# Performance work log

Measured on AMD Instinct MI355X. Metric: run time of the kernel, lower is better.

The kernel has to match this reference:

```python
import jax, jax.numpy as jnp
import numpy as np

B, M, H, R = 4096, 4, 1024, 10
MID, D3 = 512, 3 * H  # gate MLP mid = max(32, H//2)
AUDIO = 1
OTHERS = (0, 2, 3)


def _ln(x, w, b):
    m = jnp.mean(x, axis=-1, keepdims=True)
    v = jnp.mean((x - m) ** 2, axis=-1, keepdims=True)
    return (x - m) * jax.lax.rsqrt(v + 1e-5) * w + b


def _gate(t, s, lw, lb, w1, b1, w2, b2):
    feat = jnp.concatenate([t, s, jnp.abs(t - s)], axis=-1)  # [..., 3H]
    h = jax.nn.gelu(_ln(feat, lw, lb) @ w1.T + b1, approximate=False)
    return jax.nn.sigmoid(h @ w2.T + b2)  # [..., 1]


def setup_inputs() -> dict:
    key = jax.random.key(0)
    ks = jax.random.split(key, 16)
    xn = lambda k, shp, fan: jax.random.normal(k, shp, jnp.float32) * (1.0 / np.sqrt(fan))
    inp = {
        'tokens': jax.random.normal(ks[0], (B, M, H), jnp.float32),
        'token_mask': jax.random.randint(ks[1], (B, M), 0, 2) > 0,
        # gate_other: LayerNorm(3H) -> Linear(3H,MID) -> GELU -> Linear(MID,1)
        'ln_go_w': jnp.ones((D3,), jnp.float32), 'ln_go_b': jnp.zeros((D3,), jnp.float32),
        'go_w1': xn(ks[2], (MID, D3), D3), 'go_b1': jnp.zeros((MID,), jnp.float32),
        'go_w2': xn(ks[3], (1, MID), MID), 'go_b2': jnp.zeros((1,), jnp.float32),
        # gate_audio
        'ln_ga_w': jnp.ones((D3,), jnp.float32), 'ln_ga_b': jnp.zeros((D3,), jnp.float32),
        'ga_w1': xn(ks[4], (MID, D3), D3), 'ga_b1': jnp.zeros((MID,), jnp.float32),
        'ga_w2': xn(ks[5], (1, MID), MID), 'ga_b2': jnp.zeros((1,), jnp.float32),
        'a2o_w': xn(ks[6], (H, H), H), 'o2a_w': xn(ks[7], (H, H), H),
        'ln_o_w': jnp.ones((H,), jnp.float32), 'ln_o_b': jnp.zeros((H,), jnp.float32),
        'ln_a_w': jnp.ones((H,), jnp.float32), 'ln_a_b': jnp.zeros((H,), jnp.float32),
        # LMF
        'factors': jax.random.normal(ks[8], (M, R, H + 1, H), jnp.float32) * np.sqrt(2.0 / (H + 1 + H)),
        'rank_w': jax.random.normal(ks[9], (R,), jnp.float32) * 0.02,
        'lmf_bias': jnp.zeros((H,), jnp.float32),
        'out_ln1_w': jnp.ones((H,), jnp.float32), 'out_ln1_b': jnp.zeros((H,), jnp.float32),
        'out_w': xn(ks[10], (H, H), H), 'out_b': jnp.zeros((H,), jnp.float32),
        'out_ln2_w': jnp.ones((H,), jnp.float32), 'out_ln2_b': jnp.zeros((H,), jnp.float32),
    }
    return inp


def reference(tokens, token_mask, ln_go_w, ln_go_b, go_w1, go_b1, go_w2, go_b2,
              ln_ga_w, ln_ga_b, ga_w1, ga_b1, ga_w2, ga_b2, a2o_w, o2a_w,
              ln_o_w, ln_o_b, ln_a_w, ln_a_b, factors, rank_w, lmf_bias,
              out_ln1_w, out_ln1_b, out_w, out_b, out_ln2_w, out_ln2_b):
    mask_f = token_mask.astype(tokens.dtype)  # [B, M]
    oidx = jnp.asarray(OTHERS)

    # ---- AudioGuidedResidualMixer (eval mode) ----
    audio = tokens[:, AUDIO]                          # [B, H]
    audio_valid = token_mask[:, AUDIO]                # [B]
    others = tokens[:, oidx] * mask_f[:, oidx, None]  # [B, 3, H] (masked targets)
    src = jnp.broadcast_to(audio[:, None, :], others.shape)
    g = _gate(others, src, ln_go_w, ln_go_b, go_w1, go_b1, go_w2, go_b2)  # [B,3,1]
    a2o = audio @ a2o_w.T                                                  # [B, H]
    upd = _ln(others + g * a2o[:, None, :], ln_o_w, ln_o_b)
    pair_valid = token_mask[:, oidx] & audio_valid[:, None]                # [B, 3]
    others_new = jnp.where(pair_valid[..., None], upd, others) * mask_f[:, oidx, None]

    w_o = mask_f[:, oidx, None]
    denom = jnp.clip(w_o.sum(axis=1), 1.0, None)
    others_mean = (others_new * w_o).sum(axis=1) / denom                   # [B, H]
    aum = audio_valid & token_mask[:, oidx].any(axis=1)                    # [B]
    g_a = _gate(audio, others_mean, ln_ga_w, ln_ga_b, ga_w1, ga_b1, ga_w2, ga_b2)
    o2a = others_mean @ o2a_w.T
    mixed_audio = jnp.where(aum[:, None],
                            _ln(audio + g_a * o2a, ln_a_w, ln_a_b),
                            audio * mask_f[:, AUDIO, None])
    mixed = jnp.stack([others_new[:, 0], mixed_audio, others_new[:, 1], others_new[:, 2]],
                      axis=1) * mask_f[..., None]                          # [B, M, H]

    # ---- LowRankMultiplicativeFusion ----
    one = jnp.ones((mixed.shape[0], M, 1), mixed.dtype)
    x_aug = jnp.concatenate([one, mixed], axis=-1)                         # [B, M, H+1]
    z = jnp.einsum('bmd,mrdh->bmrh', x_aug, factors)                       # [B, M, R, H]
    z = jnp.where(token_mask[:, :, None, None], z, jnp.ones((), z.dtype))
    rank_tensor = jnp.prod(z, axis=1)                                      # [B, R, H]
    fused = jnp.einsum('brh,r->bh', rank_tensor, rank_w) + lmf_bias
    h = _ln(fused, out_ln1_w, out_ln1_b)
    h = jax.nn.gelu(h @ out_w.T + out_b, approximate=False)
    return _ln(h, out_ln2_w, out_ln2_b)                                    # [B, H]
```

## Files before the change

### kernel.cpp

```cpp
#include <hip/hip_runtime.h>
#include <math.h>

#define BB 4096
#define HH 1024
#define RR 10
#define MIDD 512
#define D3 3072

typedef __bf16 bf16x8 __attribute__((ext_vector_type(8)));
typedef __bf16 bf16x4 __attribute__((ext_vector_type(4)));
typedef float f32x4 __attribute__((ext_vector_type(4)));

__device__ __forceinline__ float waveSum(float v){
#pragma unroll
  for(int o=32;o>0;o>>=1) v += __shfl_down(v,o,64);
  return v;
}
__device__ __forceinline__ float blockSum256(float v, float* sc){
  v = waveSum(v);
  __syncthreads();
  if((threadIdx.x & 63)==0) sc[threadIdx.x>>6] = v;
  __syncthreads();
  return sc[0]+sc[1]+sc[2]+sc[3];
}
__device__ __forceinline__ float gelu_f(float x){
  return 0.5f*x*(1.0f+erff(x*0.70710678118654752f));
}
__device__ __forceinline__ void gl_lds16(const void* g, void* lds){
  __builtin_amdgcn_global_load_lds((const __attribute__((address_space(1))) unsigned int*)g,
                                   (__attribute__((address_space(3))) unsigned int*)lds,
                                   16, 0, 0);
}

__global__ void convw_k(const float* __restrict__ s0, __bf16* __restrict__ d0, int n0,
                        const float* __restrict__ s1, __bf16* __restrict__ d1, int n1,
                        const float* __restrict__ s2, __bf16* __restrict__ d2, int n2,
                        const float* __restrict__ s3, __bf16* __restrict__ d3, int n3,
                        const float* __restrict__ s4, __bf16* __restrict__ d4, int n4){
  long i = ((long)blockIdx.x*256 + threadIdx.x)*4;
  const float* s; __bf16* d;
  if(i<n0){ s=s0; d=d0; }
  else { i-=n0; if(i<n1){ s=s1; d=d1; }
  else { i-=n1; if(i<n2){ s=s2; d=d2; }
  else { i-=n2; if(i<n3){ s=s3; d=d3; }
  else { i-=n3; if(i>=n4) return; s=s4; d=d4; } } } }
  float4 v=*(const float4*)(s+i);
  bf16x4 o; o[0]=(__bf16)v.x; o[1]=(__bf16)v.y; o[2]=(__bf16)v.z; o[3]=(__bf16)v.w;
  *(bf16x4*)(d+i)=o;
}

__global__ void feat_go_k(const float* __restrict__ tokens, const int* __restrict__ mask,
                          const float* __restrict__ lnw, const float* __restrict__ lnb,
                          __bf16* __restrict__ featGo, __bf16* __restrict__ audioB){
  int row=blockIdx.x; int b=row/3; int j=row-b*3; int oj=(j==0)?0:(j+1);
  const float* to=tokens+((size_t)b*4+oj)*HH;
  const float* ta=tokens+((size_t)b*4+1)*HH;
  float mo = mask[b*4+oj]?1.f:0.f;
  int tid=threadIdx.x;
  __shared__ float sc[4];
  float ov[4], av[4], dv[4]; float s=0.f,s2=0.f;
#pragma unroll
  for(int p=0;p<4;p++){
    int h=tid+p*256;
    float o=to[h]*mo, a=ta[h], d=fabsf(o-a);
    ov[p]=o; av[p]=a; dv[p]=d;
    s+=o+a+d; s2+=o*o+a*a+d*d;
  }
  s=blockSum256(s,sc); s2=blockSum256(s2,sc);
  float mean=s/(float)D3, rstd=rsqrtf(s2/(float)D3-mean*mean+1e-5f);
  __bf16* fr = featGo + (size_t)row*D3;
#pragma unroll
  for(int p=0;p<4;p++){
    int h=tid+p*256;
    fr[h]       =(__bf16)((ov[p]-mean)*rstd*lnw[h]+lnb[h]);
    fr[1024+h]  =(__bf16)((av[p]-mean)*rstd*lnw[1024+h]+lnb[1024+h]);
    fr[2048+h]  =(__bf16)((dv[p]-mean)*rstd*lnw[2048+h]+lnb[2048+h]);
    if(j==0) audioB[(size_t)b*HH+h]=(__bf16)av[p];
  }
}

__global__ void feat_ga_k(const float* __restrict__ tokens, const float* __restrict__ omean,
                          const float* __restrict__ lnw, const float* __restrict__ lnb,
                          __bf16* __restrict__ featGa){
  int b=blockIdx.x; int tid=threadIdx.x;
  const float* ta=tokens+((size_t)b*4+1)*HH;
  const float* so=omean+(size_t)b*HH;
  __shared__ float sc[4];
  float tv[4], sv[4], dv[4]; float s=0.f,s2=0.f;
#pragma unroll
  for(int p=0;p<4;p++){
    int h=tid+p*256;
    float a=ta[h], o=so[h], d=fabsf(a-o);
    tv[p]=a; sv[p]=o; dv[p]=d;
    s+=a+o+d; s2+=a*a+o*o+d*d;
  }
  s=blockSum256(s,sc); s2=blockSum256(s2,sc);
  float mean=s/(float)D3, rstd=rsqrtf(s2/(float)D3-mean*mean+1e-5f);
  __bf16* fr = featGa + (size_t)b*D3;
#pragma unroll
  for(int p=0;p<4;p++){
    int h=tid+p*256;
    fr[h]     =(__bf16)((tv[p]-mean)*rstd*lnw[h]+lnb[h]);
    fr[1024+h]=(__bf16)((sv[p]-mean)*rstd*lnw[1024+h]+lnb[1024+h]);
    fr[2048+h]=(__bf16)((dv[p]-mean)*rstd*lnw[2048+h]+lnb[2048+h]);
  }
}

template<int ACT>
__launch_bounds__(256, 4)
__global__ void gemm_nt_mfma(const __bf16* __restrict__ A, int lda,
                             const __bf16* __restrict__ Bm, int ldb,
                             const float* __restrict__ bias,
                             float* __restrict__ C, int ldc, int K){
  __shared__ __align__(16) __bf16 As[3*2048];
  __shared__ __align__(16) __bf16 Bs[3*4096];
  const int tid=threadIdx.x, l=tid&63, w=tid>>6;
  const int wr=w>>1, wc=w&1;
  const int quad=l>>4, lr16=l&15;

  const int nbx = gridDim.x;
  const int flat = blockIdx.x + nbx*blockIdx.y;
  const int chunk = (nbx*gridDim.y)>>3;
  const int nid = (flat&7)*chunk + (flat>>3);
  const int bx = nid % nbx, by = nid / nbx;
  const int row0=by*64, col0=bx*128;

  const int srow=l>>2, sq=(l&3)^((l>>3)&3);
  const int nsteps = K>>5;

  const __bf16* pa  = A  + (size_t)(row0 + w*16       + srow)*lda + sq*8;
  const __bf16* pb0 = Bm + (size_t)(col0 + w*16       + srow)*ldb + sq*8;
  const __bf16* pb1 = Bm + (size_t)(col0 + (w+4)*16   + srow)*ldb + sq*8;
  __bf16* da  = As + ((size_t)w*64     + l)*8;
  __bf16* db0 = Bs + ((size_t)w*64     + l)*8;
  __bf16* db1 = Bs + ((size_t)(w+4)*64 + l)*8;

  auto stage=[&](int s,int bi){
    int k0 = s*32;
    gl_lds16(pa  + k0, da  + bi*2048);
    gl_lds16(pb0 + k0, db0 + bi*4096);
    gl_lds16(pb1 + k0, db1 + bi*4096);
  };

  f32x4 acc[2][4];
  f32x4 zerov={0.f,0.f,0.f,0.f};
#pragma unroll
  for(int i=0;i<2;i++)
#pragma unroll
    for(int j=0;j<4;j++) acc[i][j]=zerov;

  stage(0,0);
  stage(1,1);
  asm volatile("s_waitcnt vmcnt(3)" ::: "memory");
  __builtin_amdgcn_s_barrier();

  int cur=0;
  for(int step=0; step<nsteps; ++step){
    const __bf16* Ab = As + cur*2048;
    const __bf16* Bb = Bs + cur*4096;
    bf16x8 af[2], bg[4];
#pragma unroll
    for(int fi=0;fi<2;fi++){
      int R = wr*32 + fi*16 + lr16;
      af[fi]=*(const bf16x8*)(Ab + R*32 + ((quad^(R>>1))&3)*8);
    }
#pragma unroll
    for(int fj=0;fj<4;fj++){
      int N = wc*64 + fj*16 + lr16;
      bg[fj]=*(const bf16x8*)(Bb + N*32 + ((quad^(N>>1))&3)*8);
    }
    if(step+2<nsteps){
      int bi = cur + 2; if(bi>=3) bi-=3;
      stage(step+2, bi);
    }
    __builtin_amdgcn_s_setprio(1);
#pragma unroll
    for(int fi=0;fi<2;fi++)
#pragma unroll
      for(int fj=0;fj<4;fj++)
        acc[fi][fj]=__builtin_amdgcn_mfma_f32_16x16x32_bf16(af[fi],bg[fj],acc[fi][fj],0,0,0);
    __builtin_amdgcn_s_setprio(0);
    asm volatile("s_waitcnt lgkmcnt(0)" ::: "memory");
    if(step < nsteps-2) asm volatile("s_waitcnt vmcnt(3)" ::: "memory");
    else                asm volatile("s_waitcnt vmcnt(0)" ::: "memory");
    __builtin_amdgcn_s_barrier();
    cur = (cur+1==3)?0:cur+1;
  }

  float bv[4];
#pragma unroll
  for(int fj=0;fj<4;fj++) bv[fj] = (ACT==1)? bias[col0+wc*64+fj*16+lr16] : 0.f;
#pragma unroll
  for(int fi=0;fi<2;fi++){
#pragma unroll
    for(int reg=0;reg<4;reg++){
      int row=row0+wr*32+fi*16+quad*4+reg;
#pragma unroll
      for(int fj=0;fj<4;fj++){
        int col=col0+wc*64+fj*16+lr16;
        float v=acc[fi][fj][reg];
        if(ACT==1) v=gelu_f(v+bv[fj]);
        C[(size_t)row*ldc+col]=v;
      }
    }
  }
}

__global__ void gate_reduce_k(const float* __restrict__ Hx, const float* __restrict__ w2,
                              const float* __restrict__ b2, float* __restrict__ g, int cols){
  int row=blockIdx.x;
  float s=0.f;
  for(int c=threadIdx.x;c<cols;c+=64) s += Hx[(size_t)row*cols+c]*w2[c];
  s=waveSum(s);
  if(threadIdx.x==0) g[row]=1.f/(1.f+expf(-(s+b2[0])));
}

__global__ void others_k(const float* __restrict__ tokens, const int* __restrict__ mask,
                         const float* __restrict__ g, const float* __restrict__ a2o,
                         const float* __restrict__ lnw, const float* __restrict__ lnb,
                         __bf16* __restrict__ mixedB, float* __restrict__ omean,
                         __bf16* __restrict__ omeanB){
  int b=blockIdx.x, tid=threadIdx.x;
  __shared__ float sc[4];
  float ma = mask[b*4+1]?1.f:0.f;
  float a2[4];
#pragma unroll
  for(int p=0;p<4;p++) a2[p]=a2o[(size_t)b*HH+tid+p*256];
  float sum[4]={0,0,0,0}; float cnt=0.f;
  for(int j=0;j<3;j++){
    int oj=(j==0)?0:(j+1);
    float mo=mask[b*4+oj]?1.f:0.f; cnt+=mo;
    float gv=g[b*3+j];
    float t[4], ov[4]; float s=0.f,s2=0.f;
#pragma unroll
    for(int p=0;p<4;p++){
      int h=tid+p*256;
      float o=tokens[((size_t)b*4+oj)*HH+h]*mo;
      ov[p]=o; t[p]=o+gv*a2[p];
      s+=t[p]; s2+=t[p]*t[p];
    }
    s=blockSum256(s,sc); s2=blockSum256(s2,sc);
    float mean=s/1024.f, rstd=rsqrtf(s2/1024.f-mean*mean+1e-5f);
    float pv=mo*ma;
#pragma unroll
    for(int p=0;p<4;p++){
      int h=tid+p*256;
      float upd=(t[p]-mean)*rstd*lnw[h]+lnb[h];
      float on=((pv>0.5f)?upd:ov[p])*mo;
      mixedB[(size_t)b*4096 + (size_t)oj*HH + h]=(__bf16)on;
      sum[p]+=on*mo;
    }
  }
  float denom=fmaxf(cnt,1.f);
#pragma unroll
  for(int p=0;p<4;p++){
    float v=sum[p]/denom;
    omean[(size_t)b*HH+tid+p*256]=v;
    omeanB[(size_t)b*HH+tid+p*256]=(__bf16)v;
  }
}

__global__ void audio_k(const float* __restrict__ tokens, const int* __restrict__ mask,
                        const float* __restrict__ g_a, const float* __restrict__ o2a,
                        const float* __restrict__ lnw, const float* __restrict__ lnb,
                        __bf16* __restrict__ mixedB){
  int b=blockIdx.x, tid=threadIdx.x;
  __shared__ float sc[4];
  int ma_i=mask[b*4+1];
  int any = mask[b*4+0]|mask[b*4+2]|mask[b*4+3];
  bool aum = (ma_i!=0) && (any!=0);
  float ma = ma_i?1.f:0.f;
  float gv=g_a[b];
  const float* ta = tokens + ((size_t)b*4+1)*HH;
  float av[4], t[4]; float s=0.f,s2=0.f;
#pragma unroll
  for(int p=0;p<4;p++){
    int h=tid+p*256;
    av[p]=ta[h];
    t[p]=av[p]+gv*o2a[(size_t)b*HH+h];
    s+=t[p]; s2+=t[p]*t[p];
  }
  s=blockSum256(s,sc); s2=blockSum256(s2,sc);
  float mean=s/1024.f, rstd=rsqrtf(s2/1024.f-mean*mean+1e-5f);
#pragma unroll
  for(int p=0;p<4;p++){
    int h=tid+p*256;
    float u=(t[p]-mean)*rstd*lnw[h]+lnb[h];
    float outv = aum ? u : av[p]*ma;
    mixedB[(size_t)b*4096 + HH + h]=(__bf16)(outv*ma);
  }
}

__global__ void transpose_factors_k(const float* __restrict__ factors,
                                    __bf16* __restrict__ factT){
  __shared__ float T[64][65];
  int mr = blockIdx.z;
  int d0 = blockIdx.y*64, h0 = blockIdx.x*64;
  int t = threadIdx.x;
  int rr = t>>4, cc = (t&15)*4;
  const float* src = factors + ((size_t)mr*1025 + 1 + d0)*1024 + h0;
#pragma unroll
  for(int q=0;q<4;q++){
    float4 v = *(const float4*)(src + (size_t)(q*16+rr)*1024 + cc);
    T[q*16+rr][cc]=v.x; T[q*16+rr][cc+1]=v.y; T[q*16+rr][cc+2]=v.z; T[q*16+rr][cc+3]=v.w;
  }
  __syncthreads();
  __bf16* dst = factT + ((size_t)mr*1024 + h0)*1024 + d0;
#pragma unroll
  for(int q=0;q<4;q++){
    int hr = q*16 + rr;
    bf16x4 o;
    o[0]=(__bf16)T[cc][hr];   o[1]=(__bf16)T[cc+1][hr];
    o[2]=(__bf16)T[cc+2][hr]; o[3]=(__bf16)T[cc+3][hr];
    *(bf16x4*)(dst + (size_t)hr*1024 + cc) = o;
  }
}

__launch_bounds__(256, 2)
__global__ void gemm_lmf_mfma(const __bf16* __restrict__ mixedB,
                              const __bf16* __restrict__ factT,
                              const float* __restrict__ factors,
                              const int* __restrict__ mask,
                              float* __restrict__ P){
  __shared__ __align__(16) __bf16 As[3*4096];
  __shared__ __align__(16) __bf16 Bs[3*4096];
  __shared__ float Mskf[4][128];
  __shared__ float F0s[4][128];
  const int tid = threadIdx.x;
  const int l = tid & 63, w = tid >> 6;
  const int wr = w >> 1, wc = w & 1;
  const int quad = l >> 4, lr16 = l & 15;

  const int flat = blockIdx.x + 8*(blockIdx.y + 32*blockIdx.z);
  const int nid  = (flat & 7)*320 + (flat >> 3);
  const int bx   = nid & 7;
  const int rest = nid >> 3;
  const int by   = rest & 31;
  const int r    = rest >> 5;
  const int row0 = by * 128, col0 = bx * 128;

  const int srow = l >> 2;
  const int sq   = (l & 3) ^ ((l >> 3) & 3);

  for(int i = tid; i < 512; i += 256){
    int mm = i >> 7, rl = i & 127;
    Mskf[mm][rl] = mask[(row0 + rl)*4 + mm] ? 1.f : 0.f;
    F0s[mm][rl]  = factors[(size_t)(mm*RR + r)*1025*1024 + col0 + rl];
  }

  const __bf16* pa0 = mixedB + (size_t)(row0 + w*16     + srow)*4096 + sq*8;
  const __bf16* pa1 = mixedB + (size_t)(row0 + (w+4)*16 + srow)*4096 + sq*8;
  const __bf16* pb0 = factT + ((size_t)r*1024 + col0 + w*16     + srow)*1024 + sq*8;
  const __bf16* pb1 = factT + ((size_t)r*1024 + col0 + (w+4)*16 + srow)*1024 + sq*8;
  __bf16* da0 = As + ((size_t)w*64     + l)*8;
  __bf16* da1 = As + ((size_t)(w+4)*64 + l)*8;
  __bf16* db0 = Bs + ((size_t)w*64     + l)*8;
  __bf16* db1 = Bs + ((size_t)(w+4)*64 + l)*8;

  auto stage = [&](int s, int bi){
    int mm = s >> 5; int k0 = (s & 31)*32;
    size_t ao = (size_t)mm*1024 + k0;
    size_t bo = (size_t)mm*(RR*1048576) + k0;
    gl_lds16(pa0 + ao, da0 + bi*4096);
    gl_lds16(pa1 + ao, da1 + bi*4096);
    gl_lds16(pb0 + bo, db0 + bi*4096);
    gl_lds16(pb1 + bo, db1 + bi*4096);
  };

  f32x4 prod[4][4];
  f32x4 onev = {1.f,1.f,1.f,1.f};
#pragma unroll
  for(int i=0;i<4;i++)
#pragma unroll
    for(int j=0;j<4;j++) prod[i][j] = onev;

  stage(0, 0);
  stage(1, 1);
  asm volatile("s_waitcnt vmcnt(4)" ::: "memory");
  asm volatile("s_waitcnt lgkmcnt(0)" ::: "memory");
  __builtin_amdgcn_s_barrier();

  f32x4 acc[4][4];
  int cur = 0;
  for(int step = 0; step < 128; ++step){
    const __bf16* Ab = As + cur*4096;
    const __bf16* Bb = Bs + cur*4096;
    bf16x8 af[4], bg[4];
#pragma unroll
    for(int fi=0;fi<4;fi++){
      int R = wr*64 + fi*16 + lr16;
      af[fi] = *(const bf16x8*)(Ab + R*32 + ((quad ^ (R>>1)) & 3)*8);
    }
#pragma unroll
    for(int fj=0;fj<4;fj++){
      int N = wc*64 + fj*16 + lr16;
      bg[fj] = *(const bf16x8*)(Bb + N*32 + ((quad ^ (N>>1)) & 3)*8);
    }
    if(step + 2 < 128){
      int bi = cur + 2; if(bi >= 3) bi -= 3;
      stage(step + 2, bi);
    }
    if((step & 31) == 0){
      int mm = step >> 5;
#pragma unroll
      for(int fj=0;fj<4;fj++){
        float f0 = F0s[mm][wc*64 + fj*16 + lr16];
        f32x4 iv = {f0,f0,f0,f0};
#pragma unroll
        for(int fi=0;fi<4;fi++) acc[fi][fj] = iv;
      }
    }
    __builtin_amdgcn_s_setprio(1);
#pragma unroll
    for(int fi=0;fi<4;fi++)
#pragma unroll
      for(int fj=0;fj<4;fj++)
        acc[fi][fj] = __builtin_amdgcn_mfma_f32_16x16x32_bf16(af[fi], bg[fj], acc[fi][fj], 0,0,0);
    __builtin_amdgcn_s_setprio(0);
    if((step & 31) == 31){
      int mm = step >> 5;
#pragma unroll
      for(int fi=0;fi<4;fi++)
#pragma unroll
        for(int reg=0;reg<4;reg++){
          float mk = Mskf[mm][wr*64 + fi*16 + quad*4 + reg];
#pragma unroll
          for(int fj=0;fj<4;fj++)
            prod[fi][fj][reg] *= (mk != 0.f) ? acc[fi][fj][reg] : 1.f;
        }
    }
    asm volatile("s_waitcnt lgkmcnt(0)" ::: "memory");
    if(step < 126) asm volatile("s_waitcnt vmcnt(4)" ::: "memory");
    else           asm volatile("s_waitcnt vmcnt(0)" ::: "memory");
    __builtin_amdgcn_s_barrier();
    cur = (cur + 1 == 3) ? 0 : cur + 1;
  }

#pragma unroll
  for(int fi=0;fi<4;fi++){
#pragma unroll
    for(int reg=0;reg<4;reg++){
      int row = row0 + wr*64 + fi*16 + quad*4 + reg;
#pragma unroll
      for(int fj=0;fj<4;fj++){
        int col = col0 + wc*64 + fj*16 + lr16;
        P[((size_t)row*RR + r)*HH + col] = prod[fi][fj][reg];
      }
    }
  }
}

__global__ void fuse_ln_k(const float* __restrict__ P, const float* __restrict__ rank_w,
                          const float* __restrict__ lmf_bias,
                          const float* __restrict__ w, const float* __restrict__ bb,
                          __bf16* __restrict__ Y){
  int b=blockIdx.x, tid=threadIdx.x;
  __shared__ float sc[4];
  float rw[RR];
#pragma unroll
  for(int r=0;r<RR;r++) rw[r]=rank_w[r];
  const float* Pb = P + (size_t)b*RR*HH;
  float t[4]; float s=0.f,s2=0.f;
#pragma unroll
  for(int p=0;p<4;p++){
    int h=tid+p*256;
    float v=lmf_bias[h];
#pragma unroll
    for(int r=0;r<RR;r++) v += rw[r]*Pb[(size_t)r*HH+h];
    t[p]=v; s+=v; s2+=v*v;
  }
  s=blockSum256(s,sc); s2=blockSum256(s2,sc);
  float mean=s/1024.f, rstd=rsqrtf(s2/1024.f-mean*mean+1e-5f);
#pragma unroll
  for(int p=0;p<4;p++){
    int h=tid+p*256;
    Y[(size_t)b*HH+h]=(__bf16)((t[p]-mean)*rstd*w[h]+bb[h]);
  }
}

__global__ void ln_row_k(const float* __restrict__ X, const float* __restrict__ w,
                         const float* __restrict__ bb, float* __restrict__ Y){
  int b=blockIdx.x, tid=threadIdx.x;
  __shared__ float sc[4];
  const float* x=X+(size_t)b*HH;
  float t[4]; float s=0.f,s2=0.f;
#pragma unroll
  for(int p=0;p<4;p++){ t[p]=x[tid+p*256]; s+=t[p]; s2+=t[p]*t[p]; }
  s=blockSum256(s,sc); s2=blockSum256(s2,sc);
  float mean=s/1024.f, rstd=rsqrtf(s2/1024.f-mean*mean+1e-5f);
#pragma unroll
  for(int p=0;p<4;p++){
    int h=tid+p*256;
    Y[(size_t)b*HH+h]=(t[p]-mean)*rstd*w[h]+bb[h];
  }
}

extern "C" void kernel_launch(void* const* d_in, const int* in_sizes, int n_in,
                              void* d_out, int out_size, void* d_ws, size_t ws_size,
                              hipStream_t stream) {
  const float* tokens   =(const float*)d_in[0];
  const int*   mask     =(const int*)  d_in[1];
  const float* ln_go_w  =(const float*)d_in[2];
  const float* ln_go_b  =(const float*)d_in[3];
  const float* go_w1    =(const float*)d_in[4];
  const float* go_b1    =(const float*)d_in[5];
  const float* go_w2    =(const float*)d_in[6];
  const float* go_b2    =(const float*)d_in[7];
  const float* ln_ga_w  =(const float*)d_in[8];
  const float* ln_ga_b  =(const float*)d_in[9];
  const float* ga_w1    =(const float*)d_in[10];
  const float* ga_b1    =(const float*)d_in[11];
  const float* ga_w2    =(const float*)d_in[12];
  const float* ga_b2    =(const float*)d_in[13];
  const float* a2o_w    =(const float*)d_in[14];
  const float* o2a_w    =(const float*)d_in[15];
  const float* ln_o_w   =(const float*)d_in[16];
  const float* ln_o_b   =(const float*)d_in[17];
  const float* ln_a_w   =(const float*)d_in[18];
  const float* ln_a_b   =(const float*)d_in[19];
  const float* factors  =(const float*)d_in[20];
  const float* rank_w   =(const float*)d_in[21];
  const float* lmf_bias =(const float*)d_in[22];
  const float* out_ln1_w=(const float*)d_in[23];
  const float* out_ln1_b=(const float*)d_in[24];
  const float* out_w    =(const float*)d_in[25];
  const float* out_b    =(const float*)d_in[26];
  const float* out_ln2_w=(const float*)d_in[27];
  const float* out_ln2_b=(const float*)d_in[28];
  float* out=(float*)d_out;

  char* wsp=(char*)d_ws; size_t off=0;
  auto alloc=[&](size_t bytes)->void*{
    void* p=wsp+off; off=(off+bytes+255)&~(size_t)255; return p;
  };
  float*  P       =(float*) alloc((size_t)BB*RR*HH*4);
  __bf16* factT   =(__bf16*)alloc((size_t)4*RR*HH*HH*2);
  float*  H1      =(float*) alloc((size_t)BB*3*MIDD*4);
  float*  g_go    =(float*) alloc((size_t)BB*3*4);
  float*  a2o     =(float*) alloc((size_t)BB*HH*4);
  __bf16* mixedB  =(__bf16*)alloc((size_t)BB*4*HH*2);
  float*  omean   =(float*) alloc((size_t)BB*HH*4);
  __bf16* omeanB  =(__bf16*)alloc((size_t)BB*HH*2);
  __bf16* audioB  =(__bf16*)alloc((size_t)BB*HH*2);
  float*  H2      =(float*) alloc((size_t)BB*MIDD*4);
  float*  g_a     =(float*) alloc((size_t)BB*4);
  float*  o2a     =(float*) alloc((size_t)BB*HH*4);
  float*  fused   =(float*) alloc((size_t)BB*HH*4);
  __bf16* hbufB   =(__bf16*)alloc((size_t)BB*HH*2);
  __bf16* go_w1B  =(__bf16*)alloc((size_t)MIDD*D3*2);
  __bf16* ga_w1B  =(__bf16*)alloc((size_t)MIDD*D3*2);
  __bf16* a2o_wB  =(__bf16*)alloc((size_t)HH*HH*2);
  __bf16* o2a_wB  =(__bf16*)alloc((size_t)HH*HH*2);
  __bf16* out_wB  =(__bf16*)alloc((size_t)HH*HH*2);
  __bf16* featGo  =(__bf16*)P;
  __bf16* featGa  =(__bf16*)((char*)P + (size_t)BB*3*D3*2);

  {
    int n0=MIDD*D3, n1=MIDD*D3, n2=HH*HH, n3=HH*HH, n4=HH*HH;
    int total4=(n0+n1+n2+n3+n4)/4;
    convw_k<<<(total4+255)/256,256,0,stream>>>(go_w1,go_w1B,n0, ga_w1,ga_w1B,n1,
                                               a2o_w,a2o_wB,n2, o2a_w,o2a_wB,n3,
                                               out_w,out_wB,n4);
  }
  transpose_factors_k<<<dim3(16,16,40),256,0,stream>>>(factors,factT);
  feat_go_k<<<BB*3,256,0,stream>>>(tokens,mask,ln_go_w,ln_go_b,featGo,audioB);
  gemm_nt_mfma<0><<<dim3(8,64),256,0,stream>>>(audioB,HH,a2o_wB,HH,nullptr,a2o,HH,HH);
  gemm_nt_mfma<1><<<dim3(4,192),256,0,stream>>>(featGo,D3,go_w1B,D3,go_b1,H1,MIDD,D3);
  gate_reduce_k<<<BB*3,64,0,stream>>>(H1,go_w2,go_b2,g_go,MIDD);
  others_k<<<BB,256,0,stream>>>(tokens,mask,g_go,a2o,ln_o_w,ln_o_b,mixedB,omean,omeanB);
  feat_ga_k<<<BB,256,0,stream>>>(tokens,omean,ln_ga_w,ln_ga_b,featGa);
  gemm_nt_mfma<1><<<dim3(4,64),256,0,stream>>>(featGa,D3,ga_w1B,D3,ga_b1,H2,MIDD,D3);
  gate_reduce_k<<<BB,64,0,stream>>>(H2,ga_w2,ga_b2,g_a,MIDD);
  gemm_nt_mfma<0><<<dim3(8,64),256,0,stream>>>(omeanB,HH,o2a_wB,HH,nullptr,o2a,HH,HH);
  audio_k<<<BB,256,0,stream>>>(tokens,mask,g_a,o2a,ln_a_w,ln_a_b,mixedB);
  gemm_lmf_mfma<<<dim3(HH/128,BB/128,RR),256,0,stream>>>(mixedB,factT,factors,mask,P);
  fuse_ln_k<<<BB,256,0,stream>>>(P,rank_w,lmf_bias,out_ln1_w,out_ln1_b,hbufB);
  gemm_nt_mfma<1><<<dim3(8,64),256,0,stream>>>(hbufB,HH,out_wB,HH,out_b,fused,HH,HH);
  ln_row_k<<<BB,256,0,stream>>>(fused,out_ln2_w,out_ln2_b,out);
}
```

Measured before the change: 1.031 ms.

## Fuse gate reductions into GEMM epilogues and rank-sum into LMF GEMM

The gate MLP second layer (GELU, dot with w2) moves into the first GEMM's epilogue and is accumulated with atomics, which removes the H1/H2 intermediates and the gate_reduce kernels. The feat_ga construction is folded into others_k, and the LMF GEMM now processes 5 ranks per block, accumulating the rank-weighted product into fused via atomics. This drops the large P buffer and the fuse_ln kernel. In exchange the LMF grid shrinks from 2560 to 512 blocks with much longer per-block loops, and float atomics make results nondeterministic.

```diff
diff --git a/kernel.cpp b/kernel.cpp
--- a/kernel.cpp
+++ b/kernel.cpp
@@ -51,8 +51,10 @@
 
 __global__ void feat_go_k(const float* __restrict__ tokens, const int* __restrict__ mask,
                           const float* __restrict__ lnw, const float* __restrict__ lnb,
-                          __bf16* __restrict__ featGo, __bf16* __restrict__ audioB){
+                          __bf16* __restrict__ featGo, __bf16* __restrict__ audioB,
+                          float* __restrict__ gpre){
   int row=blockIdx.x; int b=row/3; int j=row-b*3; int oj=(j==0)?0:(j+1);
+  if(threadIdx.x==0) gpre[row]=0.f;
   const float* to=tokens+((size_t)b*4+oj)*HH;
   const float* ta=tokens+((size_t)b*4+1)*HH;
   float mo = mask[b*4+oj]?1.f:0.f;
@@ -79,39 +81,14 @@
   }
 }
 
-__global__ void feat_ga_k(const float* __restrict__ tokens, const float* __restrict__ omean,
-                          const float* __restrict__ lnw, const float* __restrict__ lnb,
-                          __bf16* __restrict__ featGa){
-  int b=blockIdx.x; int tid=threadIdx.x;
-  const float* ta=tokens+((size_t)b*4+1)*HH;
-  const float* so=omean+(size_t)b*HH;
-  __shared__ float sc[4];
-  float tv[4], sv[4], dv[4]; float s=0.f,s2=0.f;
-#pragma unroll
-  for(int p=0;p<4;p++){
-    int h=tid+p*256;
-    float a=ta[h], o=so[h], d=fabsf(a-o);
-    tv[p]=a; sv[p]=o; dv[p]=d;
-    s+=a+o+d; s2+=a*a+o*o+d*d;
-  }
-  s=blockSum256(s,sc); s2=blockSum256(s2,sc);
-  float mean=s/(float)D3, rstd=rsqrtf(s2/(float)D3-mean*mean+1e-5f);
-  __bf16* fr = featGa + (size_t)b*D3;
-#pragma unroll
-  for(int p=0;p<4;p++){
-    int h=tid+p*256;
-    fr[h]     =(__bf16)((tv[p]-mean)*rstd*lnw[h]+lnb[h]);
-    fr[1024+h]=(__bf16)((sv[p]-mean)*rstd*lnw[1024+h]+lnb[1024+h]);
-    fr[2048+h]=(__bf16)((dv[p]-mean)*rstd*lnw[2048+h]+lnb[2048+h]);
-  }
-}
-
 template<int ACT>
 __launch_bounds__(256, 4)
 __global__ void gemm_nt_mfma(const __bf16* __restrict__ A, int lda,
                              const __bf16* __restrict__ Bm, int ldb,
                              const float* __restrict__ bias,
-                             float* __restrict__ C, int ldc, int K){
+                             float* __restrict__ C, int ldc, int K,
+                             const float* __restrict__ w2,
+                             float* __restrict__ gpre){
   __shared__ __align__(16) __bf16 As[3*2048];
   __shared__ __align__(16) __bf16 Bs[3*4096];
   const int tid=threadIdx.x, l=tid&63, w=tid>>6;
@@ -187,6 +164,30 @@
     cur = (cur+1==3)?0:cur+1;
   }
 
+  if(ACT==2){
+    float b1v[4], w2v[4];
+#pragma unroll
+    for(int fj=0;fj<4;fj++){
+      int col=col0+wc*64+fj*16+lr16;
+      b1v[fj]=bias[col]; w2v[fj]=w2[col];
+    }
+#pragma unroll
+    for(int fi=0;fi<2;fi++){
+#pragma unroll
+      for(int reg=0;reg<4;reg++){
+        float part=0.f;
+#pragma unroll
+        for(int fj=0;fj<4;fj++) part += gelu_f(acc[fi][fj][reg]+b1v[fj])*w2v[fj];
+        part += __shfl_xor(part,1,64);
+        part += __shfl_xor(part,2,64);
+        part += __shfl_xor(part,4,64);
+        part += __shfl_xor(part,8,64);
+        if((l&15)==0) atomicAdd(&gpre[row0+wr*32+fi*16+quad*4+reg], part);
+      }
+    }
+    return;
+  }
+
   float bv[4];
 #pragma unroll
   for(int fj=0;fj<4;fj++) bv[fj] = (ACT==1)? bias[col0+wc*64+fj*16+lr16] : 0.f;
@@ -206,22 +207,16 @@
   }
 }
 
-__global__ void gate_reduce_k(const float* __restrict__ Hx, const float* __restrict__ w2,
-                              const float* __restrict__ b2, float* __restrict__ g, int cols){
-  int row=blockIdx.x;
-  float s=0.f;
-  for(int c=threadIdx.x;c<cols;c+=64) s += Hx[(size_t)row*cols+c]*w2[c];
-  s=waveSum(s);
-  if(threadIdx.x==0) g[row]=1.f/(1.f+expf(-(s+b2[0])));
-}
-
 __global__ void others_k(const float* __restrict__ tokens, const int* __restrict__ mask,
-                         const float* __restrict__ g, const float* __restrict__ a2o,
+                         const float* __restrict__ gpre, const float* __restrict__ go_b2,
+                         const float* __restrict__ a2o,
                          const float* __restrict__ lnw, const float* __restrict__ lnb,
-                         __bf16* __restrict__ mixedB, float* __restrict__ omean,
-                         __bf16* __restrict__ omeanB){
+                         const float* __restrict__ galnw, const float* __restrict__ galnb,
+                         __bf16* __restrict__ mixedB, __bf16* __restrict__ omeanB,
+                         __bf16* __restrict__ featGa, float* __restrict__ gapre){
   int b=blockIdx.x, tid=threadIdx.x;
   __shared__ float sc[4];
+  if(tid==0) gapre[b]=0.f;
   float ma = mask[b*4+1]?1.f:0.f;
   float a2[4];
 #pragma unroll
@@ -230,7 +225,7 @@
   for(int j=0;j<3;j++){
     int oj=(j==0)?0:(j+1);
     float mo=mask[b*4+oj]?1.f:0.f; cnt+=mo;
-    float gv=g[b*3+j];
+    float gv=1.f/(1.f+expf(-(gpre[b*3+j]+go_b2[0])));
     float t[4], ov[4]; float s=0.f,s2=0.f;
 #pragma unroll
     for(int p=0;p<4;p++){
@@ -252,25 +247,46 @@
     }
   }
   float denom=fmaxf(cnt,1.f);
-#pragma unroll
-  for(int p=0;p<4;p++){
-    float v=sum[p]/denom;
-    omean[(size_t)b*HH+tid+p*256]=v;
-    omeanB[(size_t)b*HH+tid+p*256]=(__bf16)v;
+  float vm[4];
+#pragma unroll
+  for(int p=0;p<4;p++){
+    vm[p]=sum[p]/denom;
+    omeanB[(size_t)b*HH+tid+p*256]=(__bf16)vm[p];
+  }
+  const float* ta=tokens+((size_t)b*4+1)*HH;
+  float tv[4], dv[4]; float s=0.f,s2=0.f;
+#pragma unroll
+  for(int p=0;p<4;p++){
+    int h=tid+p*256;
+    float a=ta[h], d=fabsf(a-vm[p]);
+    tv[p]=a; dv[p]=d;
+    s+=a+vm[p]+d; s2+=a*a+vm[p]*vm[p]+d*d;
+  }
+  s=blockSum256(s,sc); s2=blockSum256(s2,sc);
+  float mean=s/(float)D3, rstd=rsqrtf(s2/(float)D3-mean*mean+1e-5f);
+  __bf16* fr=featGa+(size_t)b*D3;
+#pragma unroll
+  for(int p=0;p<4;p++){
+    int h=tid+p*256;
+    fr[h]     =(__bf16)((tv[p]-mean)*rstd*galnw[h]+galnb[h]);
+    fr[1024+h]=(__bf16)((vm[p]-mean)*rstd*galnw[1024+h]+galnb[1024+h]);
+    fr[2048+h]=(__bf16)((dv[p]-mean)*rstd*galnw[2048+h]+galnb[2048+h]);
   }
 }
 
 __global__ void audio_k(const float* __restrict__ tokens, const int* __restrict__ mask,
-                        const float* __restrict__ g_a, const float* __restrict__ o2a,
+                        const float* __restrict__ gapre, const float* __restrict__ ga_b2,
+                        const float* __restrict__ o2a,
                         const float* __restrict__ lnw, const float* __restrict__ lnb,
-                        __bf16* __restrict__ mixedB){
+                        __bf16* __restrict__ mixedB,
+                        const float* __restrict__ lmf_bias, float* __restrict__ fused){
   int b=blockIdx.x, tid=threadIdx.x;
   __shared__ float sc[4];
   int ma_i=mask[b*4+1];
   int any = mask[b*4+0]|mask[b*4+2]|mask[b*4+3];
   bool aum = (ma_i!=0) && (any!=0);
   float ma = ma_i?1.f:0.f;
-  float gv=g_a[b];
+  float gv=1.f/(1.f+expf(-(gapre[b]+ga_b2[0])));
   const float* ta = tokens + ((size_t)b*4+1)*HH;
   float av[4], t[4]; float s=0.f,s2=0.f;
 #pragma unroll
@@ -288,6 +304,7 @@
     float u=(t[p]-mean)*rstd*lnw[h]+lnb[h];
     float outv = aum ? u : av[p]*ma;
     mixedB[(size_t)b*4096 + HH + h]=(__bf16)(outv*ma);
+    fused[(size_t)b*HH + h]=lmf_bias[h];
   }
 }
 
@@ -317,27 +334,30 @@
 }
 
 __launch_bounds__(256, 2)
-__global__ void gemm_lmf_mfma(const __bf16* __restrict__ mixedB,
-                              const __bf16* __restrict__ factT,
-                              const float* __restrict__ factors,
-                              const int* __restrict__ mask,
-                              float* __restrict__ P){
+__global__ void gemm_lmf2(const __bf16* __restrict__ mixedB,
+                          const __bf16* __restrict__ factT,
+                          const float* __restrict__ factors,
+                          const int* __restrict__ mask,
+                          const float* __restrict__ rank_w,
+                          float* __restrict__ fused){
   __shared__ __align__(16) __bf16 As[3*4096];
   __shared__ __align__(16) __bf16 Bs[3*4096];
   __shared__ float Mskf[4][128];
-  __shared__ float F0s[4][128];
+  __shared__ float F0s[20][128];
+  __shared__ float Rws[5];
   const int tid = threadIdx.x;
   const int l = tid & 63, w = tid >> 6;
   const int wr = w >> 1, wc = w & 1;
   const int quad = l >> 4, lr16 = l & 15;
 
   const int flat = blockIdx.x + 8*(blockIdx.y + 32*blockIdx.z);
-  const int nid  = (flat & 7)*320 + (flat >> 3);
-  const int bx   = nid & 7;
-  const int rest = nid >> 3;
-  const int by   = rest & 31;
-  const int r    = rest >> 5;
-  const int row0 = by * 128, col0 = bx * 128;
+  const int nid  = (flat & 7)*64 + (flat >> 3);
+  const int hh   = nid >> 6;
+  const int rest = nid & 63;
+  const int by   = rest >> 1;
+  const int bz   = rest & 1;
+  const int row0 = by * 128, col0 = hh * 128;
+  const int z5   = bz * 5;
 
   const int srow = l >> 2;
   const int sq   = (l & 3) ^ ((l >> 3) & 3);
@@ -345,34 +365,42 @@
   for(int i = tid; i < 512; i += 256){
     int mm = i >> 7, rl = i & 127;
     Mskf[mm][rl] = mask[(row0 + rl)*4 + mm] ? 1.f : 0.f;
-    F0s[mm][rl]  = factors[(size_t)(mm*RR + r)*1025*1024 + col0 + rl];
-  }
+  }
+  for(int i = tid; i < 2560; i += 256){
+    int rm = i >> 7, cl = i & 127;
+    int m = rm & 3, rg = z5 + (rm >> 2);
+    F0s[rm][cl] = factors[(size_t)(m*RR + rg)*1025*1024 + col0 + cl];
+  }
+  if(tid < 5) Rws[tid] = rank_w[z5 + tid];
 
   const __bf16* pa0 = mixedB + (size_t)(row0 + w*16     + srow)*4096 + sq*8;
   const __bf16* pa1 = mixedB + (size_t)(row0 + (w+4)*16 + srow)*4096 + sq*8;
-  const __bf16* pb0 = factT + ((size_t)r*1024 + col0 + w*16     + srow)*1024 + sq*8;
-  const __bf16* pb1 = factT + ((size_t)r*1024 + col0 + (w+4)*16 + srow)*1024 + sq*8;
+  const __bf16* pb0 = factT + ((size_t)(col0 + w*16     + srow))*1024 + sq*8;
+  const __bf16* pb1 = factT + ((size_t)(col0 + (w+4)*16 + srow))*1024 + sq*8;
   __bf16* da0 = As + ((size_t)w*64     + l)*8;
   __bf16* da1 = As + ((size_t)(w+4)*64 + l)*8;
   __bf16* db0 = Bs + ((size_t)w*64     + l)*8;
   __bf16* db1 = Bs + ((size_t)(w+4)*64 + l)*8;
 
   auto stage = [&](int s, int bi){
-    int mm = s >> 5; int k0 = (s & 31)*32;
-    size_t ao = (size_t)mm*1024 + k0;
-    size_t bo = (size_t)mm*(RR*1048576) + k0;
+    int rm = s >> 5, k0 = (s & 31)*32;
+    int m = rm & 3, rg = z5 + (rm >> 2);
+    size_t ao = (size_t)m*1024 + k0;
+    size_t bo = (size_t)(m*RR + rg)*1048576 + k0;
     gl_lds16(pa0 + ao, da0 + bi*4096);
     gl_lds16(pa1 + ao, da1 + bi*4096);
     gl_lds16(pb0 + bo, db0 + bi*4096);
     gl_lds16(pb1 + bo, db1 + bi*4096);
   };
 
+  f32x4 fsum[4][4];
   f32x4 prod[4][4];
-  f32x4 onev = {1.f,1.f,1.f,1.f};
+  f32x4 acc[4][4];
+  f32x4 zerov = {0.f,0.f,0.f,0.f};
 #pragma unroll
   for(int i=0;i<4;i++)
 #pragma unroll
-    for(int j=0;j<4;j++) prod[i][j] = onev;
+    for(int j=0;j<4;j++) fsum[i][j] = zerov;
 
   stage(0, 0);
   stage(1, 1);
@@ -380,9 +408,8 @@
   asm volatile("s_waitcnt lgkmcnt(0)" ::: "memory");
   __builtin_amdgcn_s_barrier();
 
-  f32x4 acc[4][4];
   int cur = 0;
-  for(int step = 0; step < 128; ++step){
+  for(int step = 0; step < 640; ++step){
     const __bf16* Ab = As + cur*4096;
     const __bf16* Bb = Bs + cur*4096;
     bf16x8 af[4], bg[4];
@@ -396,15 +423,22 @@
       int N = wc*64 + fj*16 + lr16;
       bg[fj] = *(const bf16x8*)(Bb + N*32 + ((quad ^ (N>>1)) & 3)*8);
     }
-    if(step + 2 < 128){
+    if(step + 2 < 640){
       int bi = cur + 2; if(bi >= 3) bi -= 3;
       stage(step + 2, bi);
     }
+    if((step & 127) == 0){
+      f32x4 onev = {1.f,1.f,1.f,1.f};
+#pragma unroll
+      for(int fi=0;fi<4;fi++)
+#pragma unroll
+        for(int fj=0;fj<4;fj++) prod[fi][fj] = onev;
+    }
     if((step & 31) == 0){
-      int mm = step >> 5;
+      int rm = step >> 5;
 #pragma unroll
       for(int fj=0;fj<4;fj++){
-        float f0 = F0s[mm][wc*64 + fj*16 + lr16];
+        float f0 = F0s[rm][wc*64 + fj*16 + lr16];
         f32x4 iv = {f0,f0,f0,f0};
 #pragma unroll
         for(int fi=0;fi<4;fi++) acc[fi][fj] = iv;
@@ -418,7 +452,7 @@
         acc[fi][fj] = __builtin_amdgcn_mfma_f32_16x16x32_bf16(af[fi], bg[fj], acc[fi][fj], 0,0,0);
     __builtin_amdgcn_s_setprio(0);
     if((step & 31) == 31){
-      int mm = step >> 5;
+      int mm = (step >> 5) & 3;
 #pragma unroll
       for(int fi=0;fi<4;fi++)
 #pragma unroll
@@ -429,8 +463,18 @@
             prod[fi][fj][reg] *= (mk != 0.f) ? acc[fi][fj][reg] : 1.f;
         }
     }
+    if((step & 127) == 127){
+      float rw = Rws[step >> 7];
+#pragma unroll
+      for(int fi=0;fi<4;fi++)
+#pragma unroll
+        for(int fj=0;fj<4;fj++)
+#pragma unroll
+          for(int reg=0;reg<4;reg++)
+            fsum[fi][fj][reg] += rw * prod[fi][fj][reg];
+    }
     asm volatile("s_waitcnt lgkmcnt(0)" ::: "memory");
-    if(step < 126) asm volatile("s_waitcnt vmcnt(4)" ::: "memory");
+    if(step < 638) asm volatile("s_waitcnt vmcnt(4)" ::: "memory");
     else           asm volatile("s_waitcnt vmcnt(0)" ::: "memory");
     __builtin_amdgcn_s_barrier();
     cur = (cur + 1 == 3) ? 0 : cur + 1;
@@ -444,37 +488,9 @@
 #pragma unroll
       for(int fj=0;fj<4;fj++){
         int col = col0 + wc*64 + fj*16 + lr16;
-        P[((size_t)row*RR + r)*HH + col] = prod[fi][fj][reg];
+        atomicAdd(&fused[(size_t)row*HH + col], fsum[fi][fj][reg]);
       }
     }
-  }
-}
-
-__global__ void fuse_ln_k(const float* __restrict__ P, const float* __restrict__ rank_w,
-                          const float* __restrict__ lmf_bias,
-                          const float* __restrict__ w, const float* __restrict__ bb,
-                          __bf16* __restrict__ Y){
-  int b=blockIdx.x, tid=threadIdx.x;
-  __shared__ float sc[4];
-  float rw[RR];
-#pragma unroll
-  for(int r=0;r<RR;r++) rw[r]=rank_w[r];
-  const float* Pb = P + (size_t)b*RR*HH;
-  float t[4]; float s=0.f,s2=0.f;
-#pragma unroll
-  for(int p=0;p<4;p++){
-    int h=tid+p*256;
-    float v=lmf_bias[h];
-#pragma unroll
-    for(int r=0;r<RR;r++) v += rw[r]*Pb[(size_t)r*HH+h];
-    t[p]=v; s+=v; s2+=v*v;
-  }
-  s=blockSum256(s,sc); s2=blockSum256(s2,sc);
-  float mean=s/1024.f, rstd=rsqrtf(s2/1024.f-mean*mean+1e-5f);
-#pragma unroll
-  for(int p=0;p<4;p++){
-    int h=tid+p*256;
-    Y[(size_t)b*HH+h]=(__bf16)((t[p]-mean)*rstd*w[h]+bb[h]);
   }
 }
 
@@ -492,6 +508,22 @@
   for(int p=0;p<4;p++){
     int h=tid+p*256;
     Y[(size_t)b*HH+h]=(t[p]-mean)*rstd*w[h]+bb[h];
+  }
+}
+__global__ void ln_row_bf16_k(const float* __restrict__ X, const float* __restrict__ w,
+                              const float* __restrict__ bb, __bf16* __restrict__ Y){
+  int b=blockIdx.x, tid=threadIdx.x;
+  __shared__ float sc[4];
+  const float* x=X+(size_t)b*HH;
+  float t[4]; float s=0.f,s2=0.f;
+#pragma unroll
+  for(int p=0;p<4;p++){ t[p]=x[tid+p*256]; s+=t[p]; s2+=t[p]*t[p]; }
+  s=blockSum256(s,sc); s2=blockSum256(s2,sc);
+  float mean=s/1024.f, rstd=rsqrtf(s2/1024.f-mean*mean+1e-5f);
+#pragma unroll
+  for(int p=0;p<4;p++){
+    int h=tid+p*256;
+    Y[(size_t)b*HH+h]=(__bf16)((t[p]-mean)*rstd*w[h]+bb[h]);
   }
 }
 
@@ -533,17 +565,15 @@
   auto alloc=[&](size_t bytes)->void*{
     void* p=wsp+off; off=(off+bytes+255)&~(size_t)255; return p;
   };
-  float*  P       =(float*) alloc((size_t)BB*RR*HH*4);
   __bf16* factT   =(__bf16*)alloc((size_t)4*RR*HH*HH*2);
-  float*  H1      =(float*) alloc((size_t)BB*3*MIDD*4);
-  float*  g_go    =(float*) alloc((size_t)BB*3*4);
+  __bf16* featGo  =(__bf16*)alloc((size_t)BB*3*D3*2);
+  __bf16* featGa  =(__bf16*)alloc((size_t)BB*D3*2);
+  float*  g_go_pre=(float*) alloc((size_t)BB*3*4);
+  float*  ga_pre  =(float*) alloc((size_t)BB*4);
   float*  a2o     =(float*) alloc((size_t)BB*HH*4);
   __bf16* mixedB  =(__bf16*)alloc((size_t)BB*4*HH*2);
-  float*  omean   =(float*) alloc((size_t)BB*HH*4);
   __bf16* omeanB  =(__bf16*)alloc((size_t)BB*HH*2);
   __bf16* audioB  =(__bf16*)alloc((size_t)BB*HH*2);
-  float*  H2      =(float*) alloc((size_t)BB*MIDD*4);
-  float*  g_a     =(float*) alloc((size_t)BB*4);
   float*  o2a     =(float*) alloc((size_t)BB*HH*4);
   float*  fused   =(float*) alloc((size_t)BB*HH*4);
   __bf16* hbufB   =(__bf16*)alloc((size_t)BB*HH*2);
@@ -552,8 +582,6 @@
   __bf16* a2o_wB  =(__bf16*)alloc((size_t)HH*HH*2);
   __bf16* o2a_wB  =(__bf16*)alloc((size_t)HH*HH*2);
   __bf16* out_wB  =(__bf16*)alloc((size_t)HH*HH*2);
-  __bf16* featGo  =(__bf16*)P;
-  __bf16* featGa  =(__bf16*)((char*)P + (size_t)BB*3*D3*2);
 
   {
     int n0=MIDD*D3, n1=MIDD*D3, n2=HH*HH, n3=HH*HH, n4=HH*HH;
@@ -563,18 +591,16 @@
                                                out_w,out_wB,n4);
   }
   transpose_factors_k<<<dim3(16,16,40),256,0,stream>>>(factors,factT);
-  feat_go_k<<<BB*3,256,0,stream>>>(tokens,mask,ln_go_w,ln_go_b,featGo,audioB);
-  gemm_nt_mfma<0><<<dim3(8,64),256,0,stream>>>(audioB,HH,a2o_wB,HH,nullptr,a2o,HH,HH);
-  gemm_nt_mfma<1><<<dim3(4,192),256,0,stream>>>(featGo,D3,go_w1B,D3,go_b1,H1,MIDD,D3);
-  gate_reduce_k<<<BB*3,64,0,stream>>>(H1,go_w2,go_b2,g_go,MIDD);
-  others_k<<<BB,256,0,stream>>>(tokens,mask,g_go,a2o,ln_o_w,ln_o_b,mixedB,omean,omeanB);
-  feat_ga_k<<<BB,256,0,stream>>>(tokens,omean,ln_ga_w,ln_ga_b,featGa);
-  gemm_nt_mfma<1><<<dim3(4,64),256,0,stream>>>(featGa,D3,ga_w1B,D3,ga_b1,H2,MIDD,D3);
-  gate_reduce_k<<<BB,64,0,stream>>>(H2,ga_w2,ga_b2,g_a,MIDD);
-  gemm_nt_mfma<0><<<dim3(8,64),256,0,stream>>>(omeanB,HH,o2a_wB,HH,nullptr,o2a,HH,HH);
-  audio_k<<<BB,256,0,stream>>>(tokens,mask,g_a,o2a,ln_a_w,ln_a_b,mixedB);
-  gemm_lmf_mfma<<<dim3(HH/128,BB/128,RR),256,0,stream>>>(mixedB,factT,factors,mask,P);
-  fuse_ln_k<<<BB,256,0,stream>>>(P,rank_w,lmf_bias,out_ln1_w,out_ln1_b,hbufB);
-  gemm_nt_mfma<1><<<dim3(8,64),256,0,stream>>>(hbufB,HH,out_wB,HH,out_b,fused,HH,HH);
+  feat_go_k<<<BB*3,256,0,stream>>>(tokens,mask,ln_go_w,ln_go_b,featGo,audioB,g_go_pre);
+  gemm_nt_mfma<0><<<dim3(8,64),256,0,stream>>>(audioB,HH,a2o_wB,HH,nullptr,a2o,HH,HH,nullptr,nullptr);
+  gemm_nt_mfma<2><<<dim3(4,192),256,0,stream>>>(featGo,D3,go_w1B,D3,go_b1,nullptr,0,D3,go_w2,g_go_pre);
+  others_k<<<BB,256,0,stream>>>(tokens,mask,g_go_pre,go_b2,a2o,ln_o_w,ln_o_b,
+                                ln_ga_w,ln_ga_b,mixedB,omeanB,featGa,ga_pre);
+  gemm_nt_mfma<2><<<dim3(4,64),256,0,stream>>>(featGa,D3,ga_w1B,D3,ga_b1,nullptr,0,D3,ga_w2,ga_pre);
+  gemm_nt_mfma<0><<<dim3(8,64),256,0,stream>>>(omeanB,HH,o2a_wB,HH,nullptr,o2a,HH,HH,nullptr,nullptr);
+  audio_k<<<BB,256,0,stream>>>(tokens,mask,ga_pre,ga_b2,o2a,ln_a_w,ln_a_b,mixedB,lmf_bias,fused);
+  gemm_lmf2<<<dim3(8,32,2),256,0,stream>>>(mixedB,factT,factors,mask,rank_w,fused);
+  ln_row_bf16_k<<<BB,256,0,stream>>>(fused,out_ln1_w,out_ln1_b,hbufB);
+  gemm_nt_mfma<1><<<dim3(8,64),256,0,stream>>>(hbufB,HH,out_wB,HH,out_b,fused,HH,HH,nullptr,nullptr);
   ln_row_k<<<BB,256,0,stream>>>(fused,out_ln2_w,out_ln2_b,out);
 }
```

New measurement: 1.021 ms. No clear change (-1.0%).
